# Optimization experiments

Hardware: AMD Instinct MI355X
Metric: run time of the kernel (lower is better)

## Reference

```python
import jax, jax.numpy as jnp
import numpy as np

B, C, H, W, D = 2, 256, 16, 16, 16
HEADS, DIM_HEAD = 8, 64
HIDDEN = HEADS * DIM_HEAD  # 512
EPS = 1e-12  # torch F.normalize default eps


def setup_inputs() -> dict:
    key = jax.random.key(0)
    k1, k2, k3 = jax.random.split(key, 3)
    x = jax.random.normal(k1, (B, C, H, W, D), dtype=jnp.float32)
    g = jnp.ones((C,), dtype=jnp.float32)
    # conv 1x1 weights act as plain matrices over the channel dim
    w_qkv = jax.random.normal(k2, (3 * HIDDEN, C), dtype=jnp.float32) * (C ** -0.5)
    w_out = jax.random.normal(k3, (C, HIDDEN), dtype=jnp.float32) * (HIDDEN ** -0.5)
    b_out = jnp.zeros((C,), dtype=jnp.float32)
    return {"x": x, "g": g, "w_qkv": w_qkv, "w_out": w_out, "b_out": b_out}


def reference(x, g, w_qkv, w_out, b_out):
    b, c, h, w, d = x.shape
    n = h * w * d
    # RMSNorm3D: F.normalize(x, dim=1) * g * sqrt(C)
    norm = jnp.sqrt(jnp.sum(x * x, axis=1, keepdims=True))
    xn = x / jnp.maximum(norm, EPS) * g[None, :, None, None, None] * (c ** 0.5)
    xt = xn.reshape(b, c, n)  # [b, c, n]
    # 1x1 conv3d == channel matmul
    qkv = jnp.einsum('oc,bcn->bon', w_qkv, xt)  # [b, 3*hidden, n]
    q, k, v = jnp.split(qkv, 3, axis=1)
    def to_heads(t):  # [b, heads*dh, n] -> [b, heads, n, dh]
        return t.reshape(b, HEADS, DIM_HEAD, n).transpose(0, 1, 3, 2)
    q, k, v = to_heads(q), to_heads(k), to_heads(v)
    scale = DIM_HEAD ** -0.5
    sim = jnp.einsum('bhid,bhjd->bhij', q * scale, k)  # [b, heads, n, n]
    attn = jax.nn.softmax(sim, axis=-1)
    out = jnp.einsum('bhij,bhjd->bhid', attn, v)  # [b, heads, n, dh]
    out = out.transpose(0, 1, 3, 2).reshape(b, HIDDEN, n)  # [b, hidden, n]
    y = jnp.einsum('oc,bcn->bon', w_out, out) + b_out[None, :, None]
    return y.reshape(b, c, h, w, d)
```

## Files before the change

kernel.cpp:

```cpp
#include <hip/hip_runtime.h>
#include <type_traits>

#define DI __device__ __forceinline__

typedef __attribute__((ext_vector_type(8))) __bf16 vbf8;
typedef __attribute__((ext_vector_type(8))) short  vs8;
typedef __attribute__((ext_vector_type(4))) float  f4;
typedef __attribute__((ext_vector_type(4))) unsigned int u32x4;

static constexpr int BB   = 2;
static constexpr int C    = 256;
static constexpr int NN   = 4096;
static constexpr int HID  = 512;
static constexpr int QKVR = 1536;

static DI unsigned short f2bf(float f) {
  unsigned int u = __builtin_bit_cast(unsigned int, f);
  u += 0x7fffu + ((u >> 16) & 1u);
  return (unsigned short)(u >> 16);
}
static DI float bf2f(unsigned short u) {
  return __builtin_bit_cast(float, (unsigned int)u << 16);
}
static DI unsigned int cvtpk(float lo, float hi) {
  unsigned int r;
  asm("v_cvt_pk_bf16_f32 %0, %1, %2" : "=v"(r) : "v"(lo), "v"(hi));
  return r;
}
static DI float EXP2(float x) {
  float r;
  asm("v_exp_f32 %0, %1" : "=v"(r) : "v"(x));
  return r;
}

template <typename V>
static DI auto mfma_sel(V a, V b, f4 c, int)
    -> decltype(__builtin_amdgcn_mfma_f32_16x16x32_bf16(a, b, c, 0, 0, 0)) {
  return __builtin_amdgcn_mfma_f32_16x16x32_bf16(a, b, c, 0, 0, 0);
}
template <typename V>
static DI f4 mfma_sel(V a, V b, f4 c, long) {
  return __builtin_amdgcn_mfma_f32_16x16x32_bf16(
      __builtin_bit_cast(vs8, a), __builtin_bit_cast(vs8, b), c, 0, 0, 0);
}
static DI f4 MFMA(vs8 a, vs8 b, f4 c) {
  return mfma_sel(__builtin_bit_cast(vbf8, a), __builtin_bit_cast(vbf8, b), c, 0);
}

static DI void gll16(const unsigned short* g, unsigned short* l) {
  __builtin_amdgcn_global_load_lds(
      (const __attribute__((address_space(1))) unsigned int*)g,
      (__attribute__((address_space(3))) unsigned int*)l, 16, 0, 0);
}

__global__ void k_prep(const float* __restrict__ wqkv, const float* __restrict__ g,
                       const float* __restrict__ wout,
                       unsigned short* __restrict__ wg, unsigned short* __restrict__ wo) {
  int i = blockIdx.x * 256 + threadIdx.x;
  if (i < QKVR * C) wg[i] = f2bf(wqkv[i] * g[i & (C - 1)]);
  if (i < C * HID)  wo[i] = f2bf(wout[i]);
}

__global__ __launch_bounds__(256) void k_qkv(const float* __restrict__ x,
    const unsigned short* __restrict__ wg,
    unsigned short* __restrict__ qo, unsigned short* __restrict__ ko,
    unsigned short* __restrict__ vo) {
  __shared__ unsigned short xs[64 * 264];
  __shared__ float ps[4][64];
  __shared__ float inv[64];
  const int bo = blockIdx.x % 6;
  const int bn = (blockIdx.x / 6) & 63;
  const int b  = blockIdx.x / 384;
  const int o0 = bo * 256, n0 = bn * 64;
  const int tid = threadIdx.x;
  {
    const int nl = tid & 63, cb = tid >> 6;
    const float* xp = x + (size_t)b * C * NN + n0 + nl;
    float s = 0.f;
    #pragma unroll
    for (int k8 = 0; k8 < 8; ++k8) {
      float v[8];
      #pragma unroll
      for (int j = 0; j < 8; ++j) {
        v[j] = xp[(size_t)(cb * 64 + k8 * 8 + j) * NN];
        s += v[j] * v[j];
      }
      u32x4 pk;
      pk[0] = cvtpk(v[0], v[1]); pk[1] = cvtpk(v[2], v[3]);
      pk[2] = cvtpk(v[4], v[5]); pk[3] = cvtpk(v[6], v[7]);
      *(u32x4*)(&xs[nl * 264 + cb * 64 + k8 * 8]) = pk;
    }
    ps[cb][nl] = s;
  }
  __syncthreads();
  if (tid < 64) {
    float t4 = ps[0][tid] + ps[1][tid] + ps[2][tid] + ps[3][tid];
    inv[tid] = 16.0f / fmaxf(sqrtf(t4), 1e-12f);
  }
  __syncthreads();
  const int wave = tid >> 6, lane = tid & 63, lr = lane & 15, lg = lane >> 4;
  const int orow = o0 + wave * 64;
  f4 acc[4][4];
  #pragma unroll
  for (int om = 0; om < 4; ++om)
    #pragma unroll
    for (int nc = 0; nc < 4; ++nc) acc[om][nc] = f4{0.f, 0.f, 0.f, 0.f};
  const unsigned short* wpb = wg + (size_t)(orow + lr) * C + lg * 8;
  #pragma unroll
  for (int c0 = 0; c0 < C; c0 += 32) {
    vs8 bfv[4];
    #pragma unroll
    for (int nc = 0; nc < 4; ++nc)
      bfv[nc] = *(const vs8*)(&xs[(nc * 16 + lr) * 264 + c0 + lg * 8]);
    #pragma unroll
    for (int om = 0; om < 4; ++om) {
      vs8 af = *(const vs8*)(wpb + (size_t)om * 16 * C + c0);
      #pragma unroll
      for (int nc = 0; nc < 4; ++nc) acc[om][nc] = MFMA(af, bfv[nc], acc[om][nc]);
    }
  }
  #pragma unroll
  for (int om = 0; om < 4; ++om) {
    const int om_row = orow + om * 16;
    const int otype = om_row >> 9;
    const int head  = (om_row >> 6) & 7;
    const int bh    = b * 8 + head;
    const int dbase = (om_row & 63) + lg * 4;
    #pragma unroll
    for (int nc = 0; nc < 4; ++nc) {
      const int n = n0 + nc * 16 + lr;
      float s = inv[nc * 16 + lr];
      if (otype == 0) s *= 0.125f * 1.44269504088896f;
      if (otype < 2) {
        unsigned short* dst = (otype == 0 ? qo : ko) + ((size_t)bh * NN + n) * 64 + dbase;
        unsigned int lo = cvtpk(acc[om][nc][0] * s, acc[om][nc][1] * s);
        unsigned int hi = cvtpk(acc[om][nc][2] * s, acc[om][nc][3] * s);
        *(unsigned long long*)dst = ((unsigned long long)hi << 32) | lo;
      } else {
        const int np = n0 + ((nc >> 1) << 5) + ((lr >> 2) << 3) + ((nc & 1) << 2) + (lr & 3);
        #pragma unroll
        for (int r = 0; r < 4; ++r)
          vo[((size_t)bh * 64 + dbase + r) * NN + np] = f2bf(acc[om][nc][r] * s);
      }
    }
  }
}

template <int SPLITS>
__global__ __launch_bounds__(256, 4) void k_attn(const unsigned short* __restrict__ qq,
    const unsigned short* __restrict__ kk, const unsigned short* __restrict__ vv,
    unsigned short* __restrict__ ou, float* __restrict__ st) {
  __shared__ unsigned short stg[2][8192];
  constexpr int NB  = 512 * SPLITS;
  constexpr int CPX = NB / 8;
  constexpr int JCH = NN / SPLITS / 64;
  const int bid = blockIdx.x;
  const int swz = (bid & 7) * CPX + (bid >> 3);
  const int qt   = swz & 31;
  const int rest = swz >> 5;
  const int sp   = (SPLITS > 1) ? (rest % SPLITS) : 0;
  const int bh   = (SPLITS > 1) ? (rest / SPLITS) : rest;
  const int js   = sp * (NN / SPLITS);
  const int tid = threadIdx.x, wave = tid >> 6, lane = tid & 63;
  const int lr = lane & 15, lg = lane >> 4;
  const int qbase = qt * 128 + wave * 32;
  const unsigned short* kb = kk + (size_t)bh * NN * 64;
  const unsigned short* vb = vv + (size_t)bh * 64 * NN;
  vs8 qf[2][2];
  #pragma unroll
  for (int qn = 0; qn < 2; ++qn)
    #pragma unroll
    for (int kd = 0; kd < 2; ++kd)
      qf[qn][kd] = *(const vs8*)(qq + ((size_t)bh * NN + qbase + qn * 16 + lr) * 64 + kd * 32 + lg * 8);
  const vs8 onesf = {0x3F80, 0x3F80, 0x3F80, 0x3F80, 0x3F80, 0x3F80, 0x3F80, 0x3F80};
  const f4 zero4 = {0.f, 0.f, 0.f, 0.f};
  f4 oacc[4][2] = { { {0,0,0,0},{0,0,0,0} }, { {0,0,0,0},{0,0,0,0} },
                    { {0,0,0,0},{0,0,0,0} }, { {0,0,0,0},{0,0,0,0} } };
  f4 lacc[2] = { {0,0,0,0}, {0,0,0,0} };

  auto stage = [&](int j0, int buf) {
    #pragma unroll
    for (int p = 0; p < 2; ++p) {
      const int g  = wave * 2 + p;
      const int jt = g >> 1, kd = g & 1;
      gll16(kb + (size_t)(j0 + jt * 16 + lr) * 64 + kd * 32 + lg * 8,
            &stg[buf][g * 512]);
      const int dt = g >> 1, kj = g & 1;
      gll16(vb + (size_t)(dt * 16 + lr) * NN + j0 + kj * 32 + lg * 8,
            &stg[buf][4096 + g * 512]);
    }
  };

  stage(js, 0);
  asm volatile("s_waitcnt vmcnt(0)");
  __syncthreads();

  for (int t = 0; t < JCH; ++t) {
    const int cur = t & 1;
    if (t + 1 < JCH) stage(js + (t + 1) * 64, cur ^ 1);
    const unsigned short* sbk = stg[cur];
    const unsigned short* sbv = stg[cur] + 4096;
    f4 s[4][2];
    __builtin_amdgcn_s_setprio(1);
    #pragma unroll
    for (int jt = 0; jt < 4; ++jt) {
      vs8 k0 = *(const vs8*)(sbk + (jt * 2 + 0) * 512 + lane * 8);
      vs8 k1 = *(const vs8*)(sbk + (jt * 2 + 1) * 512 + lane * 8);
      #pragma unroll
      for (int qn = 0; qn < 2; ++qn) {
        s[jt][qn] = MFMA(k0, qf[qn][0], zero4);
        s[jt][qn] = MFMA(k1, qf[qn][1], s[jt][qn]);
      }
    }
    __builtin_amdgcn_s_setprio(0);
    vs8 pb[2][2];
    #pragma unroll
    for (int qn = 0; qn < 2; ++qn)
      #pragma unroll
      for (int kj = 0; kj < 2; ++kj) {
        u32x4 w;
        w[0] = cvtpk(EXP2(s[2 * kj][qn][0]),     EXP2(s[2 * kj][qn][1]));
        w[1] = cvtpk(EXP2(s[2 * kj][qn][2]),     EXP2(s[2 * kj][qn][3]));
        w[2] = cvtpk(EXP2(s[2 * kj + 1][qn][0]), EXP2(s[2 * kj + 1][qn][1]));
        w[3] = cvtpk(EXP2(s[2 * kj + 1][qn][2]), EXP2(s[2 * kj + 1][qn][3]));
        pb[qn][kj] = __builtin_bit_cast(vs8, w);
      }
    __builtin_amdgcn_s_setprio(1);
    #pragma unroll
    for (int kj = 0; kj < 2; ++kj) {
      #pragma unroll
      for (int mt = 0; mt < 4; ++mt) {
        vs8 vf = *(const vs8*)(sbv + (mt * 2 + kj) * 512 + lane * 8);
        oacc[mt][0] = MFMA(vf, pb[0][kj], oacc[mt][0]);
        oacc[mt][1] = MFMA(vf, pb[1][kj], oacc[mt][1]);
      }
      lacc[0] = MFMA(onesf, pb[0][kj], lacc[0]);
      lacc[1] = MFMA(onesf, pb[1][kj], lacc[1]);
    }
    __builtin_amdgcn_s_setprio(0);
    asm volatile("s_waitcnt vmcnt(0)");
    __syncthreads();
  }
  const int b = bh >> 3, h = bh & 7;
  float rl2[2] = {1.f, 1.f};
  if (SPLITS == 1) { rl2[0] = 1.0f / lacc[0][0]; rl2[1] = 1.0f / lacc[1][0]; }
  const size_t rowbase = (size_t)((SPLITS > 1 ? sp * BB : 0) + b) * NN;
  #pragma unroll
  for (int mt = 0; mt < 4; ++mt)
    #pragma unroll
    for (int qn = 0; qn < 2; ++qn) {
      unsigned int w0 = cvtpk(oacc[mt][qn][0] * rl2[qn], oacc[mt][qn][1] * rl2[qn]);
      unsigned int w1 = cvtpk(oacc[mt][qn][2] * rl2[qn], oacc[mt][qn][3] * rl2[qn]);
      const int q = qbase + qn * 16 + lr;
      *(unsigned long long*)(&ou[(rowbase + q) * HID + h * 64 + mt * 16 + lg * 4]) =
          ((unsigned long long)w1 << 32) | w0;
    }
  if (SPLITS > 1 && lg == 0) {
    #pragma unroll
    for (int qn = 0; qn < 2; ++qn)
      st[(size_t)(sp * 16 + bh) * NN + qbase + qn * 16 + lr] = lacc[qn][0];
  }
}

template <int SPLITS>
__global__ __launch_bounds__(256) void k_out(const unsigned short* __restrict__ ou,
    const float* __restrict__ st, const unsigned short* __restrict__ wo,
    const float* __restrict__ bout, float* __restrict__ y) {
  const int bo = blockIdx.x & 3;
  const int bn = (blockIdx.x >> 2) & 63;
  const int b  = blockIdx.x >> 8;
  const int o0 = bo * 64, n0 = bn * 64;
  const int tid = threadIdx.x, wave = tid >> 6, lane = tid & 63, lr = lane & 15, lg = lane >> 4;
  const int orow = o0 + wave * 16;
  f4 acc[4] = { {0,0,0,0},{0,0,0,0},{0,0,0,0},{0,0,0,0} };
  if constexpr (SPLITS == 1) {
    const unsigned short* wp = wo + (size_t)(orow + lr) * HID + lg * 8;
    const unsigned short* op = ou + ((size_t)b * NN + n0) * HID + lg * 8;
    #pragma unroll
    for (int c00 = 0; c00 < HID; c00 += 32) {
      vs8 af = *(const vs8*)(wp + c00);
      #pragma unroll
      for (int nc = 0; nc < 4; ++nc) {
        vs8 bf = *(const vs8*)(op + (size_t)(nc * 16 + lr) * HID + c00);
        acc[nc] = MFMA(af, bf, acc[nc]);
      }
    }
  } else {
    __shared__ unsigned short os[64 * 136];
    for (int c0 = 0; c0 < HID; c0 += 128) {
      __syncthreads();
      {
        const int nl = tid & 63, cb = tid >> 6;
        const int n = n0 + nl;
        const int h  = (c0 + cb * 32) >> 6;
        const int bh = b * 8 + h;
        float lsum = 0.f;
        #pragma unroll
        for (int s = 0; s < SPLITS; ++s) lsum += st[(size_t)(s * 16 + bh) * NN + n];
        const float rl = 1.0f / lsum;
        #pragma unroll
        for (int t = 0; t < 4; ++t) {
          const int cc = cb * 32 + t * 8;
          float a[8] = {0,0,0,0,0,0,0,0};
          #pragma unroll
          for (int s = 0; s < SPLITS; ++s) {
            vs8 v = *(const vs8*)(&ou[((size_t)(s * BB + b) * NN + n) * HID + c0 + cc]);
            #pragma unroll
            for (int j = 0; j < 8; ++j) a[j] += bf2f((unsigned short)v[j]);
          }
          u32x4 pk;
          pk[0] = cvtpk(a[0] * rl, a[1] * rl);
          pk[1] = cvtpk(a[2] * rl, a[3] * rl);
          pk[2] = cvtpk(a[4] * rl, a[5] * rl);
          pk[3] = cvtpk(a[6] * rl, a[7] * rl);
          *(u32x4*)(&os[nl * 136 + cc]) = pk;
        }
      }
      __syncthreads();
      const unsigned short* wp = wo + (size_t)(orow + lr) * HID + c0 + lg * 8;
      #pragma unroll
      for (int cc0 = 0; cc0 < 128; cc0 += 32) {
        vs8 af = *(const vs8*)(wp + cc0);
        #pragma unroll
        for (int nc = 0; nc < 4; ++nc) {
          vs8 bf = *(const vs8*)(&os[(nc * 16 + lr) * 136 + cc0 + lg * 8]);
          acc[nc] = MFMA(af, bf, acc[nc]);
        }
      }
    }
  }
  #pragma unroll
  for (int nc = 0; nc < 4; ++nc) {
    const int n = n0 + nc * 16 + lr;
    #pragma unroll
    for (int r = 0; r < 4; ++r)
      y[((size_t)b * C + orow + lg * 4 + r) * NN + n] = acc[nc][r] + bout[orow + lg * 4 + r];
  }
}

extern "C" void kernel_launch(void* const* d_in, const int* in_sizes, int n_in,
                              void* d_out, int out_size, void* d_ws, size_t ws_size,
                              hipStream_t stream) {
  const float* x    = (const float*)d_in[0];
  const float* g    = (const float*)d_in[1];
  const float* wqkv = (const float*)d_in[2];
  const float* wout = (const float*)d_in[3];
  const float* bout = (const float*)d_in[4];
  float* y = (float*)d_out;
  char* ws = (char*)d_ws;
  unsigned short* wg  = (unsigned short*)(ws);
  unsigned short* wo  = (unsigned short*)(ws + 786432);
  unsigned short* qb  = (unsigned short*)(ws + 1048576);
  unsigned short* kb  = (unsigned short*)(ws + 1048576 + 8388608);
  unsigned short* vtb = (unsigned short*)(ws + 1048576 + 2 * 8388608);
  unsigned short* ou  = (unsigned short*)(ws + 1048576 + 3 * 8388608);
  k_prep<<<1536, 256, 0, stream>>>(wqkv, g, wout, wg, wo);
  k_qkv<<<768, 256, 0, stream>>>(x, wg, qb, kb, vtb);
  k_attn<1><<<512, 256, 0, stream>>>(qb, kb, vtb, ou, nullptr);
  k_out<1><<<512, 256, 0, stream>>>(ou, nullptr, wo, bout, y);
}
```

Before: 120.7 us.

## Split RMSNorm into separate kernel producing pre-normalized bf16 tiles for QKV GEMM

Adds a k_xn kernel that reads each x tile once, computes the RMS norm and writes normalized bf16 data in an MFMA-friendly tiled layout. Before this, k_qkv re-read and transposed the fp32 x tile six times, once per output block. k_qkv now loads the tile with global_load_lds and drops the norm scaling. The split-K attention template path is also removed as dead code. The cost is an extra launch and an extra 4MB workspace round trip, and k_xn runs only 128 blocks.

```diff
diff --git a/kernel.cpp b/kernel.cpp
--- a/kernel.cpp
+++ b/kernel.cpp
@@ -18,9 +18,6 @@
   unsigned int u = __builtin_bit_cast(unsigned int, f);
   u += 0x7fffu + ((u >> 16) & 1u);
   return (unsigned short)(u >> 16);
-}
-static DI float bf2f(unsigned short u) {
-  return __builtin_bit_cast(float, (unsigned int)u << 16);
 }
 static DI unsigned int cvtpk(float lo, float hi) {
   unsigned int r;
@@ -61,44 +58,69 @@
   if (i < C * HID)  wo[i] = f2bf(wout[i]);
 }
 
-__global__ __launch_bounds__(256) void k_qkv(const float* __restrict__ x,
+__global__ __launch_bounds__(256) void k_xn(const float* __restrict__ x,
+                                            unsigned short* __restrict__ xn) {
+  __shared__ float xsf[64 * 257];
+  __shared__ float ps[4][64];
+  __shared__ float inv[64];
+  const int bn = blockIdx.x & 63, b = blockIdx.x >> 6;
+  const int n0 = bn * 64;
+  const int tid = threadIdx.x;
+  const int nl = tid & 63, cb = tid >> 6;
+  {
+    const float* xp = x + (size_t)b * C * NN + n0 + nl;
+    float s = 0.f;
+    #pragma unroll 8
+    for (int k = 0; k < 64; ++k) {
+      int c = cb * 64 + k;
+      float v = xp[(size_t)c * NN];
+      s += v * v;
+      xsf[nl * 257 + c] = v;
+    }
+    ps[cb][nl] = s;
+  }
+  __syncthreads();
+  if (tid < 64) {
+    float t4 = ps[0][tid] + ps[1][tid] + ps[2][tid] + ps[3][tid];
+    inv[tid] = 16.0f / fmaxf(sqrtf(t4), 1e-12f);
+  }
+  __syncthreads();
+  unsigned short* out = xn + (size_t)(b * 64 + bn) * 32 * 512;
+  const float s = inv[nl];
+  #pragma unroll
+  for (int t = 0; t < 8; ++t) {
+    const int g = cb * 8 + t;
+    const float* src = &xsf[nl * 257 + g * 8];
+    u32x4 pk;
+    pk[0] = cvtpk(src[0] * s, src[1] * s);
+    pk[1] = cvtpk(src[2] * s, src[3] * s);
+    pk[2] = cvtpk(src[4] * s, src[5] * s);
+    pk[3] = cvtpk(src[6] * s, src[7] * s);
+    *(u32x4*)(&out[(size_t)g * 512 + nl * 8]) = pk;
+  }
+}
+
+__global__ __launch_bounds__(256) void k_qkv(const unsigned short* __restrict__ xn,
     const unsigned short* __restrict__ wg,
     unsigned short* __restrict__ qo, unsigned short* __restrict__ ko,
     unsigned short* __restrict__ vo) {
-  __shared__ unsigned short xs[64 * 264];
-  __shared__ float ps[4][64];
-  __shared__ float inv[64];
+  __shared__ unsigned short xs[32 * 512];
   const int bo = blockIdx.x % 6;
   const int bn = (blockIdx.x / 6) & 63;
   const int b  = blockIdx.x / 384;
   const int o0 = bo * 256, n0 = bn * 64;
-  const int tid = threadIdx.x;
+  const int tid = threadIdx.x, wave = tid >> 6, lane = tid & 63;
+  const int lr = lane & 15, lg = lane >> 4;
   {
-    const int nl = tid & 63, cb = tid >> 6;
-    const float* xp = x + (size_t)b * C * NN + n0 + nl;
-    float s = 0.f;
-    #pragma unroll
-    for (int k8 = 0; k8 < 8; ++k8) {
-      float v[8];
-      #pragma unroll
-      for (int j = 0; j < 8; ++j) {
-        v[j] = xp[(size_t)(cb * 64 + k8 * 8 + j) * NN];
-        s += v[j] * v[j];
-      }
-      u32x4 pk;
-      pk[0] = cvtpk(v[0], v[1]); pk[1] = cvtpk(v[2], v[3]);
-      pk[2] = cvtpk(v[4], v[5]); pk[3] = cvtpk(v[6], v[7]);
-      *(u32x4*)(&xs[nl * 264 + cb * 64 + k8 * 8]) = pk;
-    }
-    ps[cb][nl] = s;
-  }
+    const unsigned short* src = xn + (size_t)(b * 64 + bn) * 32 * 512;
+    #pragma unroll
+    for (int p = 0; p < 8; ++p) {
+      const int g = wave * 8 + p;
+      gll16(src + (size_t)g * 512 + lane * 8, &xs[g * 512]);
+    }
+  }
+  asm volatile("s_waitcnt vmcnt(0)");
   __syncthreads();
-  if (tid < 64) {
-    float t4 = ps[0][tid] + ps[1][tid] + ps[2][tid] + ps[3][tid];
-    inv[tid] = 16.0f / fmaxf(sqrtf(t4), 1e-12f);
-  }
-  __syncthreads();
-  const int wave = tid >> 6, lane = tid & 63, lr = lane & 15, lg = lane >> 4;
   const int orow = o0 + wave * 64;
   f4 acc[4][4];
   #pragma unroll
@@ -111,7 +133,7 @@
     vs8 bfv[4];
     #pragma unroll
     for (int nc = 0; nc < 4; ++nc)
-      bfv[nc] = *(const vs8*)(&xs[(nc * 16 + lr) * 264 + c0 + lg * 8]);
+      bfv[nc] = *(const vs8*)(&xs[((c0 >> 3) + lg) * 512 + (nc * 16 + lr) * 8]);
     #pragma unroll
     for (int om = 0; om < 4; ++om) {
       vs8 af = *(const vs8*)(wpb + (size_t)om * 16 * C + c0);
@@ -126,11 +148,10 @@
     const int head  = (om_row >> 6) & 7;
     const int bh    = b * 8 + head;
     const int dbase = (om_row & 63) + lg * 4;
+    const float s = (otype == 0) ? 0.125f * 1.44269504088896f : 1.0f;
     #pragma unroll
     for (int nc = 0; nc < 4; ++nc) {
       const int n = n0 + nc * 16 + lr;
-      float s = inv[nc * 16 + lr];
-      if (otype == 0) s *= 0.125f * 1.44269504088896f;
       if (otype < 2) {
         unsigned short* dst = (otype == 0 ? qo : ko) + ((size_t)bh * NN + n) * 64 + dbase;
         unsigned int lo = cvtpk(acc[om][nc][0] * s, acc[om][nc][1] * s);
@@ -146,21 +167,15 @@
   }
 }
 
-template <int SPLITS>
 __global__ __launch_bounds__(256, 4) void k_attn(const unsigned short* __restrict__ qq,
     const unsigned short* __restrict__ kk, const unsigned short* __restrict__ vv,
-    unsigned short* __restrict__ ou, float* __restrict__ st) {
+    unsigned short* __restrict__ ou) {
   __shared__ unsigned short stg[2][8192];
-  constexpr int NB  = 512 * SPLITS;
-  constexpr int CPX = NB / 8;
-  constexpr int JCH = NN / SPLITS / 64;
+  constexpr int JCH = NN / 64;
   const int bid = blockIdx.x;
-  const int swz = (bid & 7) * CPX + (bid >> 3);
-  const int qt   = swz & 31;
-  const int rest = swz >> 5;
-  const int sp   = (SPLITS > 1) ? (rest % SPLITS) : 0;
-  const int bh   = (SPLITS > 1) ? (rest / SPLITS) : rest;
-  const int js   = sp * (NN / SPLITS);
+  const int swz = (bid & 7) * 64 + (bid >> 3);
+  const int qt  = swz & 31;
+  const int bh  = swz >> 5;
   const int tid = threadIdx.x, wave = tid >> 6, lane = tid & 63;
   const int lr = lane & 15, lg = lane >> 4;
   const int qbase = qt * 128 + wave * 32;
@@ -191,13 +206,13 @@
     }
   };
 
-  stage(js, 0);
+  stage(0, 0);
   asm volatile("s_waitcnt vmcnt(0)");
   __syncthreads();
 
   for (int t = 0; t < JCH; ++t) {
     const int cur = t & 1;
-    if (t + 1 < JCH) stage(js + (t + 1) * 64, cur ^ 1);
+    if (t + 1 < JCH) stage((t + 1) * 64, cur ^ 1);
     const unsigned short* sbk = stg[cur];
     const unsigned short* sbv = stg[cur] + 4096;
     f4 s[4][2];
@@ -242,9 +257,8 @@
     __syncthreads();
   }
   const int b = bh >> 3, h = bh & 7;
-  float rl2[2] = {1.f, 1.f};
-  if (SPLITS == 1) { rl2[0] = 1.0f / lacc[0][0]; rl2[1] = 1.0f / lacc[1][0]; }
-  const size_t rowbase = (size_t)((SPLITS > 1 ? sp * BB : 0) + b) * NN;
+  float rl2[2] = {1.0f / lacc[0][0], 1.0f / lacc[1][0]};
+  const size_t rowbase = (size_t)b * NN;
   #pragma unroll
   for (int mt = 0; mt < 4; ++mt)
     #pragma unroll
@@ -255,17 +269,11 @@
       *(unsigned long long*)(&ou[(rowbase + q) * HID + h * 64 + mt * 16 + lg * 4]) =
           ((unsigned long long)w1 << 32) | w0;
     }
-  if (SPLITS > 1 && lg == 0) {
-    #pragma unroll
-    for (int qn = 0; qn < 2; ++qn)
-      st[(size_t)(sp * 16 + bh) * NN + qbase + qn * 16 + lr] = lacc[qn][0];
-  }
-}
-
-template <int SPLITS>
+}
+
 __global__ __launch_bounds__(256) void k_out(const unsigned short* __restrict__ ou,
-    const float* __restrict__ st, const unsigned short* __restrict__ wo,
-    const float* __restrict__ bout, float* __restrict__ y) {
+    const unsigned short* __restrict__ wo, const float* __restrict__ bout,
+    float* __restrict__ y) {
   const int bo = blockIdx.x & 3;
   const int bn = (blockIdx.x >> 2) & 63;
   const int b  = blockIdx.x >> 8;
@@ -273,60 +281,15 @@
   const int tid = threadIdx.x, wave = tid >> 6, lane = tid & 63, lr = lane & 15, lg = lane >> 4;
   const int orow = o0 + wave * 16;
   f4 acc[4] = { {0,0,0,0},{0,0,0,0},{0,0,0,0},{0,0,0,0} };
-  if constexpr (SPLITS == 1) {
-    const unsigned short* wp = wo + (size_t)(orow + lr) * HID + lg * 8;
-    const unsigned short* op = ou + ((size_t)b * NN + n0) * HID + lg * 8;
-    #pragma unroll
-    for (int c00 = 0; c00 < HID; c00 += 32) {
-      vs8 af = *(const vs8*)(wp + c00);
-      #pragma unroll
-      for (int nc = 0; nc < 4; ++nc) {
-        vs8 bf = *(const vs8*)(op + (size_t)(nc * 16 + lr) * HID + c00);
-        acc[nc] = MFMA(af, bf, acc[nc]);
-      }
-    }
-  } else {
-    __shared__ unsigned short os[64 * 136];
-    for (int c0 = 0; c0 < HID; c0 += 128) {
-      __syncthreads();
-      {
-        const int nl = tid & 63, cb = tid >> 6;
-        const int n = n0 + nl;
-        const int h  = (c0 + cb * 32) >> 6;
-        const int bh = b * 8 + h;
-        float lsum = 0.f;
-        #pragma unroll
-        for (int s = 0; s < SPLITS; ++s) lsum += st[(size_t)(s * 16 + bh) * NN + n];
-        const float rl = 1.0f / lsum;
-        #pragma unroll
-        for (int t = 0; t < 4; ++t) {
-          const int cc = cb * 32 + t * 8;
-          float a[8] = {0,0,0,0,0,0,0,0};
-          #pragma unroll
-          for (int s = 0; s < SPLITS; ++s) {
-            vs8 v = *(const vs8*)(&ou[((size_t)(s * BB + b) * NN + n) * HID + c0 + cc]);
-            #pragma unroll
-            for (int j = 0; j < 8; ++j) a[j] += bf2f((unsigned short)v[j]);
-          }
-          u32x4 pk;
-          pk[0] = cvtpk(a[0] * rl, a[1] * rl);
-          pk[1] = cvtpk(a[2] * rl, a[3] * rl);
-          pk[2] = cvtpk(a[4] * rl, a[5] * rl);
-          pk[3] = cvtpk(a[6] * rl, a[7] * rl);
-          *(u32x4*)(&os[nl * 136 + cc]) = pk;
-        }
-      }
-      __syncthreads();
-      const unsigned short* wp = wo + (size_t)(orow + lr) * HID + c0 + lg * 8;
-      #pragma unroll
-      for (int cc0 = 0; cc0 < 128; cc0 += 32) {
-        vs8 af = *(const vs8*)(wp + cc0);
-        #pragma unroll
-        for (int nc = 0; nc < 4; ++nc) {
-          vs8 bf = *(const vs8*)(&os[(nc * 16 + lr) * 136 + cc0 + lg * 8]);
-          acc[nc] = MFMA(af, bf, acc[nc]);
-        }
-      }
+  const unsigned short* wp = wo + (size_t)(orow + lr) * HID + lg * 8;
+  const unsigned short* op = ou + ((size_t)b * NN + n0) * HID + lg * 8;
+  #pragma unroll
+  for (int c00 = 0; c00 < HID; c00 += 32) {
+    vs8 af = *(const vs8*)(wp + c00);
+    #pragma unroll
+    for (int nc = 0; nc < 4; ++nc) {
+      vs8 bf = *(const vs8*)(op + (size_t)(nc * 16 + lr) * HID + c00);
+      acc[nc] = MFMA(af, bf, acc[nc]);
     }
   }
   #pragma unroll
@@ -350,12 +313,14 @@
   char* ws = (char*)d_ws;
   unsigned short* wg  = (unsigned short*)(ws);
   unsigned short* wo  = (unsigned short*)(ws + 786432);
-  unsigned short* qb  = (unsigned short*)(ws + 1048576);
-  unsigned short* kb  = (unsigned short*)(ws + 1048576 + 8388608);
-  unsigned short* vtb = (unsigned short*)(ws + 1048576 + 2 * 8388608);
-  unsigned short* ou  = (unsigned short*)(ws + 1048576 + 3 * 8388608);
+  unsigned short* xnb = (unsigned short*)(ws + 1048576);
+  unsigned short* qb  = (unsigned short*)(ws + 1048576 + 4194304);
+  unsigned short* kb  = (unsigned short*)(ws + 1048576 + 4194304 + 8388608);
+  unsigned short* vtb = (unsigned short*)(ws + 1048576 + 4194304 + 2 * 8388608);
+  unsigned short* ou  = (unsigned short*)(ws + 1048576 + 4194304 + 3 * 8388608);
   k_prep<<<1536, 256, 0, stream>>>(wqkv, g, wout, wg, wo);
-  k_qkv<<<768, 256, 0, stream>>>(x, wg, qb, kb, vtb);
-  k_attn<1><<<512, 256, 0, stream>>>(qb, kb, vtb, ou, nullptr);
-  k_out<1><<<512, 256, 0, stream>>>(ou, nullptr, wo, bout, y);
-}
+  k_xn<<<128, 256, 0, stream>>>(x, xnb);
+  k_qkv<<<768, 256, 0, stream>>>(xnb, wg, qb, kb, vtb);
+  k_attn<<<512, 256, 0, stream>>>(qb, kb, vtb, ou);
+  k_out<<<512, 256, 0, stream>>>(ou, wo, bout, y);
+}
```

Measured after the change: 123.7 us. 2.5% more time.
